# Kernel tuning notes

Hardware: AMD Instinct MI355X
Metric: run time of the kernel (lower is better)

## Reference

```python
import jax, jax.numpy as jnp
import numpy as np

N = 50000
E = 800000
IN_FEATS = 256
N_HIDDEN = 64
N_CLASSES = 40
HEADS = (4, 1)
NEG_SLOPE = 0.2  # DGL GATConv default


def gat_layer(x, src, dst, W, attn_l, attn_r, bias, n_heads, out_dim, activation):
    """One dglnn.GATConv layer (eval mode: dropout disabled).

    x: [N, F_in]; src/dst: [E] edge endpoints; W: [F_in, H*D];
    attn_l/attn_r: [H, D]; bias: [H*D]. Returns [N, H, D].
    """
    n = x.shape[0]
    z = (x @ W).reshape(n, n_heads, out_dim)            # [N, H, D]
    el = jnp.sum(z * attn_l[None], axis=-1)            # [N, H]
    er = jnp.sum(z * attn_r[None], axis=-1)            # [N, H]
    e = jax.nn.leaky_relu(el[src] + er[dst], NEG_SLOPE)  # [E, H]
    # segment softmax over incoming edges of each dst node
    m = jax.ops.segment_max(e, dst, num_segments=n)     # [N, H]
    a = jnp.exp(e - m[dst])                             # [E, H]
    s = jax.ops.segment_sum(a, dst, num_segments=n)     # [N, H]
    alpha = a / s[dst]                                  # [E, H]
    msg = alpha[:, :, None] * z[src]                    # [E, H, D]
    out = jax.ops.segment_sum(msg, dst, num_segments=n)  # [N, H, D]
    out = out + bias.reshape(1, n_heads, out_dim)
    if activation is not None:
        out = activation(out)
    return out


def setup_inputs() -> dict:
    key = jax.random.key(0)
    ks = jax.random.split(key, 12)
    H0, H1 = HEADS
    d_in1 = N_HIDDEN * H0
    def glorot(k, shape):
        fan = sum(shape[:2]) if len(shape) > 1 else shape[0]
        return jax.random.normal(k, shape, jnp.float32) * (2.0 / fan) ** 0.5
    return {
        "x": jax.random.normal(ks[0], (N, IN_FEATS), jnp.float32),
        "src": jax.random.randint(ks[1], (E,), 0, N),
        "dst": jax.random.randint(ks[2], (E,), 0, N),
        "W0": glorot(ks[3], (IN_FEATS, H0 * N_HIDDEN)),
        "attn_l0": glorot(ks[4], (H0, N_HIDDEN)),
        "attn_r0": glorot(ks[5], (H0, N_HIDDEN)),
        "bias0": jnp.zeros((H0 * N_HIDDEN,), jnp.float32),
        "W1": glorot(ks[6], (d_in1, H1 * N_CLASSES)),
        "attn_l1": glorot(ks[7], (H1, N_CLASSES)),
        "attn_r1": glorot(ks[8], (H1, N_CLASSES)),
        "bias1": jnp.zeros((H1 * N_CLASSES,), jnp.float32),
    }


def reference(x, src, dst, W0, attn_l0, attn_r0, bias0, W1, attn_l1, attn_r1, bias1):
    H0, H1 = HEADS
    # layer 0: GATConv + ELU, then flatten heads (l==0 branch)
    h = gat_layer(x, src, dst, W0, attn_l0, attn_r0, bias0,
                  H0, N_HIDDEN, jax.nn.elu)              # [N, H0, D]
    h = h.reshape(h.shape[0], -1)                        # [N, H0*D]
    # layer 1 (last): GATConv, no activation, head-mean (l==1 branch)
    h = gat_layer(h, src, dst, W1, attn_l1, attn_r1, bias1,
                  H1, N_CLASSES, None)                   # [N, H1, C]
    return h.mean(axis=1)                                # [N, C]
```

## Files before the change

kernel.cpp:

```cpp
#include <hip/hip_runtime.h>
#include <math.h>

using bf16x8 = __attribute__((ext_vector_type(8))) short;
using f32x4  = __attribute__((ext_vector_type(4))) float;

__device__ __forceinline__ unsigned short f2bf(float v) {
  unsigned int b = __float_as_uint(v);
  unsigned int r = (b + 0x7fffu + ((b >> 16) & 1u)) >> 16;
  return (unsigned short)r;
}
__device__ __forceinline__ float bf2f(unsigned short u) {
  return __uint_as_float(((unsigned int)u) << 16);
}


__global__ void pack_w_kernel(const float* __restrict__ W0f, unsigned short* __restrict__ Bp0,
                              const float* __restrict__ W1f, unsigned short* __restrict__ Bp1) {
  int idx = blockIdx.x * 256 + threadIdx.x;
  if (idx < 8192) {
    int lane = idx & 63, s = (idx >> 6) & 7, t = idx >> 9;
    int n = t * 16 + (lane & 15), quad = lane >> 4;
    unsigned short* o = Bp0 + (size_t)idx * 8;
    #pragma unroll
    for (int j = 0; j < 8; ++j) {
      int k = s * 32 + quad * 8 + j;
      o[j] = f2bf(W0f[(size_t)k * 256 + n]);
    }
  } else if (idx < 8192 + 1536) {
    int i1 = idx - 8192;
    int lane = i1 & 63, s = (i1 >> 6) & 7, t = i1 >> 9;
    int n = t * 16 + (lane & 15), quad = lane >> 4;
    unsigned short* o = Bp1 + (size_t)i1 * 8;
    #pragma unroll
    for (int j = 0; j < 8; ++j) {
      int k = s * 32 + quad * 8 + j;
      o[j] = (n < 40) ? f2bf(W1f[(size_t)k * 40 + n]) : 0;
    }
  }
}


__global__ __launch_bounds__(256) void mega1_kernel(
    const float* __restrict__ A, const unsigned short* __restrict__ Bp,
    unsigned short* __restrict__ Zb,
    const float* __restrict__ al, const float* __restrict__ arr,
    float* __restrict__ el, float* __restrict__ er, int M,
    const int* __restrict__ dst, int* __restrict__ deg, int E, int nG) {
  __shared__ unsigned short Bs[32768];
  int bx = blockIdx.x;

  if (bx >= nG) {
    int t = (bx - nG) * 256 + threadIdx.x;
    if (t < E) atomicAdd(&deg[dst[t]], 1);
    return;
  }

  int gx = bx >> 1, y = bx & 1;
  int tid = threadIdx.x;
  {
    const int4* s4 = (const int4*)(Bp + (size_t)y * 32768);
    int4* d4 = (int4*)Bs;
    #pragma unroll
    for (int i = 0; i < 16; ++i) d4[tid + i * 256] = s4[tid + i * 256];
  }
  __syncthreads();

  int wid = tid >> 6, lane = tid & 63;
  int quad = lane >> 4, col16 = lane & 15;
  int wr = wid >> 1, wc = wid & 1;
  int rowbase = gx * 128 + wr * 64;

  f32x4 acc[4][4];
  #pragma unroll
  for (int rt = 0; rt < 4; ++rt)
    #pragma unroll
    for (int ct = 0; ct < 4; ++ct) acc[rt][ct] = {0.f, 0.f, 0.f, 0.f};

  const bf16x8* BsV = (const bf16x8*)Bs;

  for (int s = 0; s < 8; ++s) {
    bf16x8 af[4];
    #pragma unroll
    for (int rt = 0; rt < 4; ++rt) {
      int m = rowbase + rt * 16 + col16;
      if (m < M) {
        const float* ap = A + (size_t)m * 256 + s * 32 + quad * 8;
        float4 a0 = *(const float4*)ap;
        float4 a1 = *(const float4*)(ap + 4);
        af[rt][0] = (short)f2bf(a0.x); af[rt][1] = (short)f2bf(a0.y);
        af[rt][2] = (short)f2bf(a0.z); af[rt][3] = (short)f2bf(a0.w);
        af[rt][4] = (short)f2bf(a1.x); af[rt][5] = (short)f2bf(a1.y);
        af[rt][6] = (short)f2bf(a1.z); af[rt][7] = (short)f2bf(a1.w);
      } else {
        #pragma unroll
        for (int j = 0; j < 8; ++j) af[rt][j] = 0;
      }
    }
    #pragma unroll
    for (int ct = 0; ct < 4; ++ct) {
      bf16x8 bf = BsV[((wc * 4 + ct) * 8 + s) * 64 + lane];
      #pragma unroll
      for (int rt = 0; rt < 4; ++rt)
        acc[rt][ct] = __builtin_amdgcn_mfma_f32_16x16x32_bf16(af[rt], bf, acc[rt][ct], 0, 0, 0);
    }
  }

  int hw = y * 2 + wc;
  float al_c[4], ar_c[4];
  #pragma unroll
  for (int ct = 0; ct < 4; ++ct) {
    int col = y * 128 + (wc * 4 + ct) * 16 + col16;
    al_c[ct] = al[col];
    ar_c[ct] = arr[col];
  }

  #pragma unroll
  for (int rt = 0; rt < 4; ++rt) {
    int row0 = rowbase + rt * 16 + quad * 4;
    #pragma unroll
    for (int r = 0; r < 4; ++r) {
      int row = row0 + r;
      if (row < M) {
        #pragma unroll
        for (int ct = 0; ct < 4; ++ct) {
          int col = y * 128 + (wc * 4 + ct) * 16 + col16;
          Zb[(size_t)row * 256 + col] = f2bf(acc[rt][ct][r]);
        }
      }
      float pe = 0.f, pr = 0.f;
      #pragma unroll
      for (int ct = 0; ct < 4; ++ct) {
        float zv = acc[rt][ct][r];
        pe += zv * al_c[ct];
        pr += zv * ar_c[ct];
      }
      pe += __shfl_xor(pe, 1); pr += __shfl_xor(pr, 1);
      pe += __shfl_xor(pe, 2); pr += __shfl_xor(pr, 2);
      pe += __shfl_xor(pe, 4); pr += __shfl_xor(pr, 4);
      pe += __shfl_xor(pe, 8); pr += __shfl_xor(pr, 8);
      if (col16 == 0 && row < M) {
        el[(size_t)row * 4 + hw] = pe;
        er[(size_t)row * 4 + hw] = pr;
      }
    }
  }
}


__global__ void block_sum_kernel(const int* __restrict__ deg, int* __restrict__ bsum, int n) {
  __shared__ int red[4];
  int t = threadIdx.x, i = blockIdx.x * 256 + t;
  int v = (i < n) ? deg[i] : 0;
  #pragma unroll
  for (int off = 32; off; off >>= 1) v += __shfl_xor(v, off);
  if ((t & 63) == 0) red[t >> 6] = v;
  __syncthreads();
  if (t == 0) bsum[blockIdx.x] = red[0] + red[1] + red[2] + red[3];
}

__global__ void scan_bsum_kernel(const int* __restrict__ bsum, int* __restrict__ boffs,
                                 int* __restrict__ offsets, int nb, int n) {
  __shared__ int tmp[1024];
  int t = threadIdx.x;
  int v = (t < nb) ? bsum[t] : 0;
  tmp[t] = v;
  __syncthreads();
  #pragma unroll
  for (int off = 1; off < 1024; off <<= 1) {
    int add = (t >= off) ? tmp[t - off] : 0;
    __syncthreads();
    tmp[t] += add;
    __syncthreads();
  }
  if (t < nb) boffs[t] = tmp[t] - v;
  if (t == 1023) offsets[n] = tmp[1023];
}

__global__ void write_offsets_kernel(const int* __restrict__ deg, const int* __restrict__ boffs,
                                     int* __restrict__ offsets, int* __restrict__ cursor, int n) {
  __shared__ int tmp[256];
  int t = threadIdx.x, i = blockIdx.x * 256 + t;
  int v = (i < n) ? deg[i] : 0;
  tmp[t] = v;
  __syncthreads();
  #pragma unroll
  for (int off = 1; off < 256; off <<= 1) {
    int add = (t >= off) ? tmp[t - off] : 0;
    __syncthreads();
    tmp[t] += add;
    __syncthreads();
  }
  if (i < n) {
    int o = boffs[blockIdx.x] + tmp[t] - v;
    offsets[i] = o;
    cursor[i] = o;
  }
}

__global__ void build_csr_kernel(const int* __restrict__ src, const int* __restrict__ dst,
                                 int* __restrict__ cursor, int* __restrict__ src_sorted, int E) {
  int e = blockIdx.x * blockDim.x + threadIdx.x;
  if (e < E) {
    int p = atomicAdd(&cursor[dst[e]], 1);
    src_sorted[p] = src[e];
  }
}


__global__ __launch_bounds__(256) void gemm1_mfma_kernel(
    const unsigned short* __restrict__ Ab, const unsigned short* __restrict__ Bp,
    unsigned short* __restrict__ Zb,
    const float* __restrict__ al, const float* __restrict__ arr,
    float* __restrict__ el, float* __restrict__ er, int M) {
  int wid = threadIdx.x >> 6, lane = threadIdx.x & 63;
  int quad = lane >> 4, col16 = lane & 15;
  int m = blockIdx.x * 64 + wid * 16 + col16;

  f32x4 acc[3];
  #pragma unroll
  for (int t = 0; t < 3; ++t) acc[t] = {0.f, 0.f, 0.f, 0.f};

  const bf16x8* BpV = (const bf16x8*)Bp;

  for (int s = 0; s < 8; ++s) {
    bf16x8 af;
    if (m < M) {
      af = *(const bf16x8*)(Ab + (size_t)m * 256 + s * 32 + quad * 8);
    } else {
      #pragma unroll
      for (int j = 0; j < 8; ++j) af[j] = 0;
    }
    #pragma unroll
    for (int t = 0; t < 3; ++t) {
      bf16x8 bf = BpV[(t * 8 + s) * 64 + lane];
      acc[t] = __builtin_amdgcn_mfma_f32_16x16x32_bf16(af, bf, acc[t], 0, 0, 0);
    }
  }

  float al_c[3], ar_c[3];
  #pragma unroll
  for (int t = 0; t < 3; ++t) {
    int col = t * 16 + col16;
    al_c[t] = (col < 40) ? al[col] : 0.f;
    ar_c[t] = (col < 40) ? arr[col] : 0.f;
  }

  int row0 = blockIdx.x * 64 + wid * 16 + quad * 4;
  #pragma unroll
  for (int r = 0; r < 4; ++r) {
    int row = row0 + r;
    if (row < M) {
      #pragma unroll
      for (int t = 0; t < 3; ++t) {
        int col = t * 16 + col16;
        if (col < 40) Zb[(size_t)row * 40 + col] = f2bf(acc[t][r]);
      }
    }
    float pe = 0.f, pr = 0.f;
    #pragma unroll
    for (int t = 0; t < 3; ++t) {
      pe += acc[t][r] * al_c[t];
      pr += acc[t][r] * ar_c[t];
    }
    pe += __shfl_xor(pe, 1); pr += __shfl_xor(pr, 1);
    pe += __shfl_xor(pe, 2); pr += __shfl_xor(pr, 2);
    pe += __shfl_xor(pe, 4); pr += __shfl_xor(pr, 4);
    pe += __shfl_xor(pe, 8); pr += __shfl_xor(pr, 8);
    if (col16 == 0 && row < M) {
      el[row] = pe;
      er[row] = pr;
    }
  }
}


__global__ __launch_bounds__(256) void agg0_kernel(
    const int* __restrict__ offs, const int* __restrict__ ssrc,
    const float* __restrict__ el, const float* __restrict__ er,
    const unsigned short* __restrict__ zb, const float* __restrict__ bias,
    unsigned short* __restrict__ outb, int n) {
  __shared__ float sW[4][16][4];
  __shared__ int   sS[4][16];
  int wid  = threadIdx.x >> 6;
  int lane = threadIdx.x & 63;
  int node = blockIdx.x * 4 + wid;
  if (node >= n) return;
  int c = lane & 3, eoff = lane >> 2;
  int half = lane >> 5, colg = lane & 31, h2 = colg >> 3;
  int s0 = offs[node], s1 = offs[node + 1];
  float er_c = er[node * 4 + c];

  float ssum = 0.f;
  float acc[8] = {0.f, 0.f, 0.f, 0.f, 0.f, 0.f, 0.f, 0.f};
  for (int base = s0; base < s1; base += 16) {
    int cnt = min(16, s1 - base);
    if (eoff < cnt) {
      int esrc = ssrc[base + eoff];
      float v = el[esrc * 4 + c] + er_c;
      v = v > 0.f ? v : 0.2f * v;
      sW[wid][eoff][c] = expf(v);
      if (c == 0) sS[wid][eoff] = esrc;
    }
    for (int j = 0; j < cnt; j += 2) {
      int jj = j + half;
      float w = (jj < cnt) ? sW[wid][jj][h2] : 0.f;
      int sn = sS[wid][(jj < cnt) ? jj : (cnt - 1)];
      ssum += w;
      bf16x8 zu = *(const bf16x8*)(zb + (size_t)sn * 256 + (colg << 3));
      #pragma unroll
      for (int i = 0; i < 8; ++i)
        acc[i] += w * bf2f((unsigned short)zu[i]);
    }
  }

  ssum += __shfl_xor(ssum, 32);
  #pragma unroll
  for (int i = 0; i < 8; ++i) acc[i] += __shfl_xor(acc[i], 32);

  float inv = (s1 > s0) ? 1.f / ssum : 0.f;
  if (half == 0) {
    const float4 b0v = *(const float4*)(bias + (colg << 3));
    const float4 b1v = *(const float4*)(bias + (colg << 3) + 4);
    float bb[8] = {b0v.x, b0v.y, b0v.z, b0v.w, b1v.x, b1v.y, b1v.z, b1v.w};
    bf16x8 u;
    #pragma unroll
    for (int i = 0; i < 8; ++i) {
      float o = acc[i] * inv + bb[i];
      o = o > 0.f ? o : expm1f(o);
      u[i] = (short)f2bf(o);
    }
    *(bf16x8*)(outb + (size_t)node * 256 + (colg << 3)) = u;
  }
}


__global__ __launch_bounds__(256) void agg1_kernel(
    const int* __restrict__ offs, const int* __restrict__ ssrc,
    const float* __restrict__ el, const float* __restrict__ er,
    const unsigned short* __restrict__ zb, const float* __restrict__ bias,
    float* __restrict__ out, int n) {
  __shared__ float sW[4][64];
  __shared__ int   sS[4][64];
  int wid  = threadIdx.x >> 6;
  int lane = threadIdx.x & 63;
  int node = blockIdx.x * 4 + wid;
  if (node >= n) return;
  int half = lane >> 5, d = lane & 31;
  int s0 = offs[node], s1 = offs[node + 1];
  float ern = er[node];

  float ssum = 0.f;
  float2 acc = make_float2(0.f, 0.f);
  for (int base = s0; base < s1; base += 64) {
    int cnt = min(64, s1 - base);
    if (lane < cnt) {
      int esrc = ssrc[base + lane];
      float v = el[esrc] + ern;
      v = v > 0.f ? v : 0.2f * v;
      sW[wid][lane] = expf(v);
      sS[wid][lane] = esrc;
    }
    for (int j = 0; j < cnt; j += 2) {
      int jj = j + half;
      float w = (jj < cnt) ? sW[wid][jj] : 0.f;
      int sn = sS[wid][(jj < cnt) ? jj : (cnt - 1)];
      ssum += w;
      if (d < 20) {
        unsigned zp = *(const unsigned*)(zb + (size_t)sn * 40 + (d << 1));
        acc.x += w * bf2f((unsigned short)(zp & 0xffffu));
        acc.y += w * bf2f((unsigned short)(zp >> 16));
      }
    }
  }

  ssum  += __shfl_xor(ssum, 32);
  acc.x += __shfl_xor(acc.x, 32);
  acc.y += __shfl_xor(acc.y, 32);

  float inv = (s1 > s0) ? 1.f / ssum : 0.f;
  if (half == 0 && d < 20) {
    float2 o;
    o.x = acc.x * inv + bias[(d << 1) + 0];
    o.y = acc.y * inv + bias[(d << 1) + 1];
    *(float2*)(out + (size_t)node * 40 + (d << 1)) = o;
  }
}


extern "C" void kernel_launch(void* const* d_in, const int* in_sizes, int n_in,
                              void* d_out, int out_size, void* d_ws, size_t ws_size,
                              hipStream_t stream) {
  const float* x   = (const float*)d_in[0];
  const int*   src = (const int*)d_in[1];
  const int*   dst = (const int*)d_in[2];
  const float* W0  = (const float*)d_in[3];
  const float* al0 = (const float*)d_in[4];
  const float* ar0 = (const float*)d_in[5];
  const float* b0  = (const float*)d_in[6];
  const float* W1  = (const float*)d_in[7];
  const float* al1 = (const float*)d_in[8];
  const float* ar1 = (const float*)d_in[9];
  const float* b1  = (const float*)d_in[10];
  float* out = (float*)d_out;

  const int N = in_sizes[0] / 256;
  const int E = in_sizes[1];
  const int NB = (N + 255) / 256;

  char* ws = (char*)d_ws;
  size_t off = 0;
  auto alloc = [&](size_t bytes) {
    void* p = ws + off;
    off = (off + bytes + 255) & ~(size_t)255;
    return p;
  };
  unsigned short* z0b = (unsigned short*)alloc((size_t)N * 256 * 2);
  unsigned short* h0b = (unsigned short*)alloc((size_t)N * 256 * 2);
  unsigned short* z1b = (unsigned short*)alloc((size_t)N * 40 * 2);
  unsigned short* w0p = (unsigned short*)alloc((size_t)16 * 8 * 64 * 8 * 2);
  unsigned short* w1p = (unsigned short*)alloc((size_t)3 * 8 * 64 * 8 * 2);
  float* el0  = (float*)alloc((size_t)N * 4 * 4);
  float* er0  = (float*)alloc((size_t)N * 4 * 4);
  float* el1  = (float*)alloc((size_t)N * 4);
  float* er1  = (float*)alloc((size_t)N * 4);
  int* deg    = (int*)alloc((size_t)N * 4);
  int* offs   = (int*)alloc((size_t)(N + 1) * 4);
  int* cursor = (int*)alloc((size_t)N * 4);
  int* bsum   = (int*)alloc((size_t)NB * 4);
  int* boffs  = (int*)alloc((size_t)NB * 4);
  int* ssrc   = (int*)alloc((size_t)E * 4);
  (void)off; (void)ws_size; (void)n_in; (void)out_size;

  const int nG = ((N + 127) / 128) * 2;
  const int nH = (E + 255) / 256;

  pack_w_kernel<<<38, 256, 0, stream>>>(W0, w0p, W1, w1p);
  hipMemsetAsync(deg, 0, (size_t)N * 4, stream);
  mega1_kernel<<<nG + nH, 256, 0, stream>>>(x, w0p, z0b, al0, ar0, el0, er0, N,
                                            dst, deg, E, nG);
  block_sum_kernel<<<NB, 256, 0, stream>>>(deg, bsum, N);
  scan_bsum_kernel<<<1, 1024, 0, stream>>>(bsum, boffs, offs, NB, N);
  write_offsets_kernel<<<NB, 256, 0, stream>>>(deg, boffs, offs, cursor, N);
  build_csr_kernel<<<nH, 256, 0, stream>>>(src, dst, cursor, ssrc, E);
  agg0_kernel<<<(N + 3) / 4, 256, 0, stream>>>(offs, ssrc, el0, er0, z0b, b0, h0b, N);
  gemm1_mfma_kernel<<<(N + 63) / 64, 256, 0, stream>>>(h0b, w1p, z1b, al1, ar1, el1, er1, N);
  agg1_kernel<<<(N + 3) / 4, 256, 0, stream>>>(offs, ssrc, el1, er1, z1b, b1, out, N);
}
```

Baseline: 337.5 us.

## Reschedule CSR build into GEMM kernel and prefetch A fragments

The degree-count atomics move from the GEMM launch into the weight-packing launch. The CSR scatter, formerly its own kernel, now runs as extra grid-stride blocks inside the layer-0 GEMM kernel, so the scatter overlaps with the MFMA work and one launch disappears. The GEMM loop also register-double-buffers the A fragments, loading and converting the next K-slice while the current MFMAs issue. Out-of-range rows are clamped instead of zeroed, which removes the per-row branch. This costs more registers and could lower occupancy.

```diff
diff --git a/kernel.cpp b/kernel.cpp
--- a/kernel.cpp
+++ b/kernel.cpp
@@ -14,9 +14,16 @@
 }
 
 
-__global__ void pack_w_kernel(const float* __restrict__ W0f, unsigned short* __restrict__ Bp0,
-                              const float* __restrict__ W1f, unsigned short* __restrict__ Bp1) {
-  int idx = blockIdx.x * 256 + threadIdx.x;
+__global__ void mega0_kernel(const float* __restrict__ W0f, unsigned short* __restrict__ Bp0,
+                             const float* __restrict__ W1f, unsigned short* __restrict__ Bp1,
+                             const int* __restrict__ dst, int* __restrict__ deg, int E) {
+  int bx = blockIdx.x;
+  if (bx >= 38) {
+    int t = (bx - 38) * 256 + threadIdx.x;
+    if (t < E) atomicAdd(&deg[dst[t]], 1);
+    return;
+  }
+  int idx = bx * 256 + threadIdx.x;
   if (idx < 8192) {
     int lane = idx & 63, s = (idx >> 6) & 7, t = idx >> 9;
     int n = t * 16 + (lane & 15), quad = lane >> 4;
@@ -40,18 +47,73 @@
 }
 
 
-__global__ __launch_bounds__(256) void mega1_kernel(
+__global__ void block_sum_kernel(const int* __restrict__ deg, int* __restrict__ bsum, int n) {
+  __shared__ int red[4];
+  int t = threadIdx.x, i = blockIdx.x * 256 + t;
+  int v = (i < n) ? deg[i] : 0;
+  #pragma unroll
+  for (int off = 32; off; off >>= 1) v += __shfl_xor(v, off);
+  if ((t & 63) == 0) red[t >> 6] = v;
+  __syncthreads();
+  if (t == 0) bsum[blockIdx.x] = red[0] + red[1] + red[2] + red[3];
+}
+
+__global__ void scan_bsum_kernel(const int* __restrict__ bsum, int* __restrict__ boffs,
+                                 int* __restrict__ offsets, int nb, int n) {
+  __shared__ int tmp[1024];
+  int t = threadIdx.x;
+  int v = (t < nb) ? bsum[t] : 0;
+  tmp[t] = v;
+  __syncthreads();
+  #pragma unroll
+  for (int off = 1; off < 1024; off <<= 1) {
+    int add = (t >= off) ? tmp[t - off] : 0;
+    __syncthreads();
+    tmp[t] += add;
+    __syncthreads();
+  }
+  if (t < nb) boffs[t] = tmp[t] - v;
+  if (t == 1023) offsets[n] = tmp[1023];
+}
+
+__global__ void write_offsets_kernel(const int* __restrict__ deg, const int* __restrict__ boffs,
+                                     int* __restrict__ offsets, int* __restrict__ cursor, int n) {
+  __shared__ int tmp[256];
+  int t = threadIdx.x, i = blockIdx.x * 256 + t;
+  int v = (i < n) ? deg[i] : 0;
+  tmp[t] = v;
+  __syncthreads();
+  #pragma unroll
+  for (int off = 1; off < 256; off <<= 1) {
+    int add = (t >= off) ? tmp[t - off] : 0;
+    __syncthreads();
+    tmp[t] += add;
+    __syncthreads();
+  }
+  if (i < n) {
+    int o = boffs[blockIdx.x] + tmp[t] - v;
+    offsets[i] = o;
+    cursor[i] = o;
+  }
+}
+
+
+__global__ __launch_bounds__(256) void mega2_kernel(
     const float* __restrict__ A, const unsigned short* __restrict__ Bp,
     unsigned short* __restrict__ Zb,
     const float* __restrict__ al, const float* __restrict__ arr,
     float* __restrict__ el, float* __restrict__ er, int M,
-    const int* __restrict__ dst, int* __restrict__ deg, int E, int nG) {
+    const int* __restrict__ src, const int* __restrict__ dst,
+    int* __restrict__ cursor, int* __restrict__ ssrc, int E, int nG, int nC) {
   __shared__ unsigned short Bs[32768];
   int bx = blockIdx.x;
 
   if (bx >= nG) {
-    int t = (bx - nG) * 256 + threadIdx.x;
-    if (t < E) atomicAdd(&deg[dst[t]], 1);
+    int stride = nC * 256;
+    for (int e = (bx - nG) * 256 + threadIdx.x; e < E; e += stride) {
+      int p = atomicAdd(&cursor[dst[e]], 1);
+      ssrc[p] = src[e];
+    }
     return;
   }
 
@@ -70,6 +132,14 @@
   int wr = wid >> 1, wc = wid & 1;
   int rowbase = gx * 128 + wr * 64;
 
+  const float* aptr[4];
+  #pragma unroll
+  for (int rt = 0; rt < 4; ++rt) {
+    int m = rowbase + rt * 16 + col16;
+    if (m > M - 1) m = M - 1;
+    aptr[rt] = A + (size_t)m * 256 + quad * 8;
+  }
+
   f32x4 acc[4][4];
   #pragma unroll
   for (int rt = 0; rt < 4; ++rt)
@@ -78,30 +148,34 @@
 
   const bf16x8* BsV = (const bf16x8*)Bs;
 
+  auto loadA = [&](bf16x8* fr, int s) {
+    #pragma unroll
+    for (int rt = 0; rt < 4; ++rt) {
+      const float* ap = aptr[rt] + s * 32;
+      float4 a0 = *(const float4*)ap;
+      float4 a1 = *(const float4*)(ap + 4);
+      fr[rt][0] = (short)f2bf(a0.x); fr[rt][1] = (short)f2bf(a0.y);
+      fr[rt][2] = (short)f2bf(a0.z); fr[rt][3] = (short)f2bf(a0.w);
+      fr[rt][4] = (short)f2bf(a1.x); fr[rt][5] = (short)f2bf(a1.y);
+      fr[rt][6] = (short)f2bf(a1.z); fr[rt][7] = (short)f2bf(a1.w);
+    }
+  };
+
+  bf16x8 afc[4];
+  loadA(afc, 0);
   for (int s = 0; s < 8; ++s) {
-    bf16x8 af[4];
-    #pragma unroll
-    for (int rt = 0; rt < 4; ++rt) {
-      int m = rowbase + rt * 16 + col16;
-      if (m < M) {
-        const float* ap = A + (size_t)m * 256 + s * 32 + quad * 8;
-        float4 a0 = *(const float4*)ap;
-        float4 a1 = *(const float4*)(ap + 4);
-        af[rt][0] = (short)f2bf(a0.x); af[rt][1] = (short)f2bf(a0.y);
-        af[rt][2] = (short)f2bf(a0.z); af[rt][3] = (short)f2bf(a0.w);
-        af[rt][4] = (short)f2bf(a1.x); af[rt][5] = (short)f2bf(a1.y);
-        af[rt][6] = (short)f2bf(a1.z); af[rt][7] = (short)f2bf(a1.w);
-      } else {
-        #pragma unroll
-        for (int j = 0; j < 8; ++j) af[rt][j] = 0;
-      }
-    }
+    bf16x8 afn[4];
+    if (s < 7) loadA(afn, s + 1);
     #pragma unroll
     for (int ct = 0; ct < 4; ++ct) {
       bf16x8 bf = BsV[((wc * 4 + ct) * 8 + s) * 64 + lane];
       #pragma unroll
       for (int rt = 0; rt < 4; ++rt)
-        acc[rt][ct] = __builtin_amdgcn_mfma_f32_16x16x32_bf16(af[rt], bf, acc[rt][ct], 0, 0, 0);
+        acc[rt][ct] = __builtin_amdgcn_mfma_f32_16x16x32_bf16(afc[rt], bf, acc[rt][ct], 0, 0, 0);
+    }
+    if (s < 7) {
+      #pragma unroll
+      for (int rt = 0; rt < 4; ++rt) afc[rt] = afn[rt];
     }
   }
 
@@ -143,66 +217,6 @@
         er[(size_t)row * 4 + hw] = pr;
       }
     }
-  }
-}
-
-
-__global__ void block_sum_kernel(const int* __restrict__ deg, int* __restrict__ bsum, int n) {
-  __shared__ int red[4];
-  int t = threadIdx.x, i = blockIdx.x * 256 + t;
-  int v = (i < n) ? deg[i] : 0;
-  #pragma unroll
-  for (int off = 32; off; off >>= 1) v += __shfl_xor(v, off);
-  if ((t & 63) == 0) red[t >> 6] = v;
-  __syncthreads();
-  if (t == 0) bsum[blockIdx.x] = red[0] + red[1] + red[2] + red[3];
-}
-
-__global__ void scan_bsum_kernel(const int* __restrict__ bsum, int* __restrict__ boffs,
-                                 int* __restrict__ offsets, int nb, int n) {
-  __shared__ int tmp[1024];
-  int t = threadIdx.x;
-  int v = (t < nb) ? bsum[t] : 0;
-  tmp[t] = v;
-  __syncthreads();
-  #pragma unroll
-  for (int off = 1; off < 1024; off <<= 1) {
-    int add = (t >= off) ? tmp[t - off] : 0;
-    __syncthreads();
-    tmp[t] += add;
-    __syncthreads();
-  }
-  if (t < nb) boffs[t] = tmp[t] - v;
-  if (t == 1023) offsets[n] = tmp[1023];
-}
-
-__global__ void write_offsets_kernel(const int* __restrict__ deg, const int* __restrict__ boffs,
-                                     int* __restrict__ offsets, int* __restrict__ cursor, int n) {
-  __shared__ int tmp[256];
-  int t = threadIdx.x, i = blockIdx.x * 256 + t;
-  int v = (i < n) ? deg[i] : 0;
-  tmp[t] = v;
-  __syncthreads();
-  #pragma unroll
-  for (int off = 1; off < 256; off <<= 1) {
-    int add = (t >= off) ? tmp[t - off] : 0;
-    __syncthreads();
-    tmp[t] += add;
-    __syncthreads();
-  }
-  if (i < n) {
-    int o = boffs[blockIdx.x] + tmp[t] - v;
-    offsets[i] = o;
-    cursor[i] = o;
-  }
-}
-
-__global__ void build_csr_kernel(const int* __restrict__ src, const int* __restrict__ dst,
-                                 int* __restrict__ cursor, int* __restrict__ src_sorted, int E) {
-  int e = blockIdx.x * blockDim.x + threadIdx.x;
-  if (e < E) {
-    int p = atomicAdd(&cursor[dst[e]], 1);
-    src_sorted[p] = src[e];
   }
 }
 
@@ -433,15 +447,15 @@
 
   const int nG = ((N + 127) / 128) * 2;
   const int nH = (E + 255) / 256;
-
-  pack_w_kernel<<<38, 256, 0, stream>>>(W0, w0p, W1, w1p);
+  const int nC = 782;
+
   hipMemsetAsync(deg, 0, (size_t)N * 4, stream);
-  mega1_kernel<<<nG + nH, 256, 0, stream>>>(x, w0p, z0b, al0, ar0, el0, er0, N,
-                                            dst, deg, E, nG);
+  mega0_kernel<<<38 + nH, 256, 0, stream>>>(W0, w0p, W1, w1p, dst, deg, E);
   block_sum_kernel<<<NB, 256, 0, stream>>>(deg, bsum, N);
   scan_bsum_kernel<<<1, 1024, 0, stream>>>(bsum, boffs, offs, NB, N);
   write_offsets_kernel<<<NB, 256, 0, stream>>>(deg, boffs, offs, cursor, N);
-  build_csr_kernel<<<nH, 256, 0, stream>>>(src, dst, cursor, ssrc, E);
+  mega2_kernel<<<nG + nC, 256, 0, stream>>>(x, w0p, z0b, al0, ar0, el0, er0, N,
+                                            src, dst, cursor, ssrc, E, nG, nC);
   agg0_kernel<<<(N + 3) / 4, 256, 0, stream>>>(offs, ssrc, el0, er0, z0b, b0, h0b, N);
   gemm1_mfma_kernel<<<(N + 63) / 64, 256, 0, stream>>>(h0b, w1p, z1b, al1, ar1, el1, er1, N);
   agg1_kernel<<<(N + 3) / 4, 256, 0, stream>>>(offs, ssrc, el1, er1, z1b, b1, out, N);
```

Result: faster. 322.4 us (-4.5%).
